# Kernel optimization log

Measured on AMD Instinct MI355X. Metric: run time of the kernel, lower is better.

The kernel has to match this reference:

```python
import jax, jax.numpy as jnp
import numpy as np

HID = 64  # GRU hidden size fixed in source: layers.GRU(64, ...)


def setup_inputs() -> dict:
    key = jax.random.key(0)
    ks = jax.random.split(key, 9)
    B, T, D, K = 128, 1024, 128, 32
    s = 0.05
    X = jax.random.normal(ks[0], (B, T, D), jnp.float32)
    mask = jnp.ones((B, T), jnp.int32)  # 1 = valid token
    # Keras GRU (reset_after=True) params
    gru_kernel = jax.random.normal(ks[1], (D, 3 * HID), jnp.float32) * s
    gru_rec_kernel = jax.random.normal(ks[2], (HID, 3 * HID), jnp.float32) * s
    gru_bias = jax.random.normal(ks[3], (2, 3 * HID), jnp.float32) * s  # [input_bias, recurrent_bias]
    # tfa.layers.CRF params: dense projection + chain kernel + boundary energies
    dense_kernel = jax.random.normal(ks[4], (HID, K), jnp.float32) * s
    dense_bias = jax.random.normal(ks[5], (K,), jnp.float32) * s
    chain_kernel = jax.random.normal(ks[6], (K, K), jnp.float32) * s
    left_boundary = jax.random.normal(ks[7], (K,), jnp.float32) * s
    right_boundary = jax.random.normal(ks[8], (K,), jnp.float32) * s
    return {"X": X, "mask": mask, "gru_kernel": gru_kernel,
            "gru_rec_kernel": gru_rec_kernel, "gru_bias": gru_bias,
            "dense_kernel": dense_kernel, "dense_bias": dense_bias,
            "chain_kernel": chain_kernel, "left_boundary": left_boundary,
            "right_boundary": right_boundary}


def gru_forward(X, mask_bool, gru_kernel, gru_rec_kernel, gru_bias):
    # Keras GRU, reset_after=True: z/r/h gate ordering, tanh/sigmoid activations.
    B, T, D = X.shape
    xproj = X @ gru_kernel + gru_bias[0]  # [B,T,3H] input projection (fused GEMM)

    def step(h, inp):
        xp, mt = inp  # xp: [B,3H], mt: [B] bool
        rec = h @ gru_rec_kernel + gru_bias[1]  # [B,3H]
        xz, xr, xh = jnp.split(xp, 3, axis=-1)
        rz, rr, rh = jnp.split(rec, 3, axis=-1)
        z = jax.nn.sigmoid(xz + rz)
        r = jax.nn.sigmoid(xr + rr)
        hh = jnp.tanh(xh + r * rh)
        hn = z * h + (1.0 - z) * hh
        hn = jnp.where(mt[:, None], hn, h)  # masked steps carry state
        return hn, hn

    h0 = jnp.zeros((B, HID), X.dtype)
    _, hs = jax.lax.scan(step, h0, (jnp.swapaxes(xproj, 0, 1), jnp.swapaxes(mask_bool, 0, 1)))
    return jnp.swapaxes(hs, 0, 1)  # [B,T,H]


def viterbi_decode(potentials, chain_kernel):
    # Max-plus DP with backpointers; potentials: [B,T,K]
    pots = jnp.swapaxes(potentials, 0, 1)  # [T,B,K]

    def fwd(score, pot_t):
        s = score[:, :, None] + chain_kernel[None]  # [B,K_from,K_to]
        bp = jnp.argmax(s, axis=1).astype(jnp.int32)  # [B,K]
        new_score = jnp.max(s, axis=1) + pot_t
        return new_score, bp

    final_score, bps = jax.lax.scan(fwd, pots[0], pots[1:])  # bps: [T-1,B,K]
    last_tag = jnp.argmax(final_score, axis=-1).astype(jnp.int32)  # [B]

    def back(tag, bp):
        prev = jnp.take_along_axis(bp, tag[:, None], axis=1)[:, 0]
        return prev, tag

    first_tag, tags = jax.lax.scan(back, last_tag, bps, reverse=True)  # tags[t] = tag at step t+1
    decoded = jnp.concatenate([first_tag[None], tags], axis=0)  # [T,B]
    return jnp.swapaxes(decoded, 0, 1)  # [B,T]


def reference(X, mask, gru_kernel, gru_rec_kernel, gru_bias,
              dense_kernel, dense_bias, chain_kernel,
              left_boundary, right_boundary):
    B, T, D = X.shape
    mask_bool = mask == 1
    hidden = gru_forward(X, mask_bool, gru_kernel, gru_rec_kernel, gru_bias)
    potentials = hidden @ dense_kernel + dense_bias  # [B,T,K] emissions
    seq_len = jnp.sum(mask, axis=1).astype(jnp.int32)  # [B]
    # Boundary energies (tfa CRF use_boundary=True): left at t=0, right at last valid step
    potentials = potentials.at[:, 0].add(left_boundary)
    potentials = potentials.at[jnp.arange(B), seq_len - 1].add(right_boundary)
    decoded = viterbi_decode(potentials, chain_kernel)  # [B,T] int32
    return decoded, potentials, seq_len, chain_kernel
```

## Files before the change

kernel.cpp:

```cpp
#include <hip/hip_runtime.h>
#include <math.h>

#define BB 128
#define TT 1024
#define DD 128
#define HH 64
#define G3 192
#define KK 32
#define CH 32

__global__ __launch_bounds__(256, 2) void xproj_kernel(const float* __restrict__ X,
                                                       const float* __restrict__ Wk,
                                                       const float* __restrict__ gbias,
                                                       float* __restrict__ xp) {
    __shared__ float Xs[64 * 132];
    __shared__ float Ws[128 * 68];
    const int tid = threadIdx.x;
    const int row0 = blockIdx.x * 64;
    const int cg = blockIdx.y;
#pragma unroll
    for (int it = 0; it < 8; ++it) {
        int idx = it * 1024 + tid * 4;
        int r = idx >> 7, c = idx & 127;
        float4 v = *(const float4*)&X[((size_t)(row0 + r)) * DD + c];
        *(float4*)&Xs[r * 132 + c] = v;
    }
#pragma unroll
    for (int it = 0; it < 8; ++it) {
        int idx = it * 1024 + tid * 4;
        int k = idx >> 6, c = idx & 63;
        float4 v = *(const float4*)&Wk[(size_t)k * G3 + cg * 64 + c];
        *(float4*)&Ws[k * 68 + c] = v;
    }
    __syncthreads();
    const int tr = tid >> 4, tc = tid & 15;
    const int r0 = tr * 4, c0 = tc * 4;
    float acc[4][4];
#pragma unroll
    for (int r = 0; r < 4; ++r)
#pragma unroll
        for (int c = 0; c < 4; ++c) acc[r][c] = 0.f;
#pragma unroll 4
    for (int k = 0; k < DD; k += 4) {
        float a[4][4];
#pragma unroll
        for (int r = 0; r < 4; ++r) {
            float4 t = *(const float4*)&Xs[(r0 + r) * 132 + k];
            a[r][0] = t.x; a[r][1] = t.y; a[r][2] = t.z; a[r][3] = t.w;
        }
#pragma unroll
        for (int kk = 0; kk < 4; ++kk) {
            float4 b = *(const float4*)&Ws[(k + kk) * 68 + c0];
#pragma unroll
            for (int r = 0; r < 4; ++r) {
                acc[r][0] += a[r][kk] * b.x;
                acc[r][1] += a[r][kk] * b.y;
                acc[r][2] += a[r][kk] * b.z;
                acc[r][3] += a[r][kk] * b.w;
            }
        }
    }
    float4 bias = *(const float4*)&gbias[cg * 64 + c0];
#pragma unroll
    for (int r = 0; r < 4; ++r) {
        float4 o;
        o.x = acc[r][0] + bias.x; o.y = acc[r][1] + bias.y;
        o.z = acc[r][2] + bias.z; o.w = acc[r][3] + bias.w;
        *(float4*)&xp[((size_t)(row0 + r0 + r)) * G3 + cg * 64 + c0] = o;
    }
}

#define BCAST(v, l) __int_as_float(__builtin_amdgcn_readlane(__float_as_int(v), (l)))

__global__ __launch_bounds__(320, 1)
void fused_kernel(const float* __restrict__ xp,
                  const float* __restrict__ Wr,
                  const float* __restrict__ gbias,
                  const int* __restrict__ mask,
                  const float* __restrict__ Dk,
                  const float* __restrict__ db,
                  const float* __restrict__ chain,
                  const float* __restrict__ lb,
                  const float* __restrict__ rb,
                  float* __restrict__ out_pot,
                  float* __restrict__ out_dec,
                  float* __restrict__ out_slen,
                  float* __restrict__ out_chn) {
    const int b = blockIdx.x;
    const int tid = threadIdx.x;
    const int w = tid >> 6;
    const int l = tid & 63;
    const int bTT = b * TT;

    __shared__ unsigned char bp[(TT - 1) * KK];
    __shared__ unsigned char table[32 * 32 * KK];
    __shared__ int ent[32];
    __shared__ int last_tag_s;
    __shared__ float gbuf[2][4 * HH];
    __shared__ __align__(16) float hbuf[4][HH];
    __shared__ __align__(16) float potring[64][KK];
    __shared__ __align__(16) float xpstage[2][CH * G3];
    __shared__ int maskst[2][CH];

    if (w < 3) {
        const int j = l;
        float wg[HH];
#pragma unroll
        for (int i2 = 0; i2 < HH; ++i2) wg[i2] = Wr[i2 * G3 + w * HH + j];
#pragma unroll
        for (int i2 = 0; i2 < HH; ++i2) asm volatile("" : "+v"(wg[i2]));
        const float bw = gbias[G3 + w * HH + j];
        __builtin_amdgcn_s_setprio(1);
        float h = 0.f;
        __syncthreads();
        float xv0 = xpstage[0][tid];
        int m0 = maskst[0][0];
        for (int i = 0; i < TT + 2; ++i) {
            if (i < TT) {
                float a0 = bw, a1 = 0.f, a2 = 0.f, a3 = 0.f;
#pragma unroll
                for (int c = 0; c < HH; c += 4) {
                    a0 += BCAST(h, c + 0) * wg[c + 0];
                    a1 += BCAST(h, c + 1) * wg[c + 1];
                    a2 += BCAST(h, c + 2) * wg[c + 2];
                    a3 += BCAST(h, c + 3) * wg[c + 3];
                }
                float a = (a0 + a1) + (a2 + a3);
                float g = (w == 2) ? a : 1.f / (1.f + __expf(-(xv0 + a)));
                gbuf[i & 1][w * HH + j] = g;
                if (w == 2) gbuf[i & 1][3 * HH + j] = xv0;
            }
            __syncthreads();
            if (i < TT) {
                float z  = gbuf[i & 1][j];
                float r  = gbuf[i & 1][HH + j];
                float rh = gbuf[i & 1][2 * HH + j];
                float xh = gbuf[i & 1][3 * HH + j];
                float y = xh + r * rh;
                float hh = 1.f - 2.f / (1.f + __expf(2.f * y));
                float hn = z * h + (1.f - z) * hh;
                hn = (m0 != 0) ? hn : h;
                h = hn;
                if (w == 0) hbuf[i & 3][j] = hn;
                if (i < TT - 1) {
                    const int t1 = i + 1;
                    xv0 = xpstage[(t1 >> 5) & 1][(t1 & 31) * G3 + tid];
                    m0  = maskst[(t1 >> 5) & 1][t1 & 31];
                }
            }
        }
    } else if (w == 3) {
        const int k = l & 31;
        int sl = 0;
#pragma unroll
        for (int q = 0; q < 16; ++q) sl += mask[bTT + q * 64 + l];
#pragma unroll
        for (int d = 32; d >= 1; d >>= 1) sl += __shfl_xor(sl, d, 64);
        if (l == 0) out_slen[b] = (float)sl;
        float dk[HH];
#pragma unroll
        for (int i2 = 0; i2 < HH; ++i2) dk[i2] = Dk[i2 * KK + k];
#pragma unroll
        for (int i2 = 0; i2 < HH; ++i2) asm volatile("" : "+v"(dk[i2]));
        const float dbk = db[k], lbk = lb[k], rbk = rb[k];
        const float* xpg = xp + (size_t)bTT * G3;
        float* potg = out_pot + (size_t)bTT * KK;
#pragma unroll
        for (int q = 0; q < 24; ++q) {
            float4 v = *(const float4*)&xpg[q * 256 + l * 4];
            *(float4*)&xpstage[0][q * 256 + l * 4] = v;
        }
        if (l < CH) maskst[0][l] = mask[bTT + l];
        __syncthreads();
        for (int i = 0; i < TT + 2; ++i) {
            if ((i & 31) == 0) {
                const int cn = (i >> 5) + 1;
                if (cn < 32) {
                    const float* src = xpg + (size_t)cn * CH * G3;
                    float* dst = &xpstage[cn & 1][0];
#pragma unroll
                    for (int q = 0; q < 24; ++q) {
                        float4 v = *(const float4*)&src[q * 256 + l * 4];
                        *(float4*)&dst[q * 256 + l * 4] = v;
                    }
                    if (l < CH) maskst[cn & 1][l] = mask[bTT + cn * CH + l];
                }
                const int cf = (i >> 5) - 2;
                if (cf >= 0) {
                    const float* srcl = &potring[(cf & 1) * 32][0];
                    float* dstg = potg + (size_t)cf * CH * KK;
#pragma unroll
                    for (int q = 0; q < 4; ++q) {
                        float4 v = *(const float4*)&srcl[q * 256 + l * 4];
                        *(float4*)&dstg[q * 256 + l * 4] = v;
                    }
                }
            }
            const int t = i - 2;
            if (t >= 0 && t < TT) {
                const float4* hv4 = (const float4*)&hbuf[t & 3][0];
                float p0 = dbk, p1 = 0.f, p2 = 0.f, p3 = 0.f;
#pragma unroll
                for (int c = 0; c < 16; ++c) {
                    float4 hv = hv4[c];
                    p0 += hv.x * dk[4 * c + 0];
                    p1 += hv.y * dk[4 * c + 1];
                    p2 += hv.z * dk[4 * c + 2];
                    p3 += hv.w * dk[4 * c + 3];
                }
                float pot = (p0 + p1) + (p2 + p3);
                if (t == 0) pot += lbk;
                if (t == sl - 1) pot += rbk;
                if (l < 32) potring[t & 63][k] = pot;
            }
            __syncthreads();
        }
        {
            const float* srcl = &potring[(31 & 1) * 32][0];
            float* dstg = potg + (size_t)31 * CH * KK;
#pragma unroll
            for (int q = 0; q < 4; ++q) {
                float4 v = *(const float4*)&srcl[q * 256 + l * 4];
                *(float4*)&dstg[q * 256 + l * 4] = v;
            }
        }
    } else {
        const int k = l & 31;
        const int hf = l >> 5;
        float ccol[16];
        int addr[16];
#pragma unroll
        for (int m = 0; m < 16; ++m) {
            ccol[m] = chain[(hf * 16 + m) * KK + k];
            addr[m] = (hf * 16 + m) * 4;
        }
#pragma unroll
        for (int m = 0; m < 16; ++m) asm volatile("" : "+v"(ccol[m]));
        const int addrx = (l ^ 32) * 4;
        float s = 0.f;
        __syncthreads();
        for (int i = 0; i < TT + 2; ++i) {
            __syncthreads();
            const int t = i - 2;
            if (t >= 0 && t < TT) {
                float pot = potring[t & 63][k];
                if (t == 0) {
                    s = pot;
                } else {
                    const int si = __float_as_int(s);
                    float c[16];
#pragma unroll
                    for (int m = 0; m < 16; ++m)
                        c[m] = __int_as_float(__builtin_amdgcn_ds_bpermute(addr[m], si)) + ccol[m];
                    float v1[8]; int i1[8];
#pragma unroll
                    for (int p = 0; p < 8; ++p) {
                        bool tk = c[2 * p + 1] > c[2 * p];
                        v1[p] = tk ? c[2 * p + 1] : c[2 * p];
                        i1[p] = hf * 16 + (tk ? 2 * p + 1 : 2 * p);
                    }
                    float v2[4]; int i2[4];
#pragma unroll
                    for (int p = 0; p < 4; ++p) {
                        bool tk = v1[2 * p + 1] > v1[2 * p];
                        v2[p] = tk ? v1[2 * p + 1] : v1[2 * p];
                        i2[p] = tk ? i1[2 * p + 1] : i1[2 * p];
                    }
                    float v3[2]; int i3[2];
#pragma unroll
                    for (int p = 0; p < 2; ++p) {
                        bool tk = v2[2 * p + 1] > v2[2 * p];
                        v3[p] = tk ? v2[2 * p + 1] : v2[2 * p];
                        i3[p] = tk ? i2[2 * p + 1] : i2[2 * p];
                    }
                    bool tk = v3[1] > v3[0];
                    float bv = tk ? v3[1] : v3[0];
                    int bi = tk ? i3[1] : i3[0];
                    float ov = __int_as_float(__builtin_amdgcn_ds_bpermute(addrx, __float_as_int(bv)));
                    int   oi = __builtin_amdgcn_ds_bpermute(addrx, bi);
                    bool take = (ov > bv) || (ov == bv && oi < bi);
                    if (take) { bv = ov; bi = oi; }
                    if (l < 32) bp[(t - 1) * KK + k] = (unsigned char)bi;
                    s = bv + pot;
                }
            }
        }
        float bv = s; int bi = k;
#pragma unroll
        for (int d = 16; d >= 1; d >>= 1) {
            float ov = __shfl_xor(bv, d, 64);
            int   oi = __shfl_xor(bi, d, 64);
            bool take = (ov > bv) || (ov == bv && oi < bi);
            if (take) { bv = ov; bi = oi; }
        }
        if (l == 0) last_tag_s = bi;
    }
    __syncthreads();
    {
        const int k = tid & 31;
        const int grp = tid >> 5;
        for (int c = grp; c < 32; c += 10) {
            int tag = k;
            for (int ll = 31; ll >= 0; --ll) {
                const int t = c * 32 + ll;
                if (t < TT - 1) tag = bp[t * KK + tag];
                table[(c * 32 + ll) * KK + k] = (unsigned char)tag;
            }
        }
    }
    __syncthreads();
    if (tid == 0) {
        int e = last_tag_s;
        ent[31] = e;
        for (int c = 30; c >= 0; --c) { e = table[(c + 1) * 32 * KK + e]; ent[c] = e; }
    }
    __syncthreads();
    for (int t = tid; t < TT; t += 320) {
        const int c = t >> 5, ll = t & 31;
        out_dec[(size_t)bTT + t] = (float)table[(c * 32 + ll) * KK + ent[c]];
    }
    if (b == 0) {
        for (int i2 = tid; i2 < KK * KK; i2 += 320) out_chn[i2] = chain[i2];
    }
}

extern "C" void kernel_launch(void* const* d_in, const int* in_sizes, int n_in,
                              void* d_out, int out_size, void* d_ws, size_t ws_size,
                              hipStream_t stream) {
    const float* X     = (const float*)d_in[0];
    const int*   mask  = (const int*)d_in[1];
    const float* Wk    = (const float*)d_in[2];
    const float* Wr    = (const float*)d_in[3];
    const float* gb    = (const float*)d_in[4];
    const float* Dk    = (const float*)d_in[5];
    const float* db    = (const float*)d_in[6];
    const float* chain = (const float*)d_in[7];
    const float* lb    = (const float*)d_in[8];
    const float* rb    = (const float*)d_in[9];

    float* out = (float*)d_out;
    float* out_dec  = out;
    float* out_pot  = out + (size_t)BB * TT;
    float* out_slen = out + (size_t)BB * TT + (size_t)BB * TT * KK;
    float* out_chn  = out_slen + BB;

    float* xp = (float*)d_ws;

    xproj_kernel<<<dim3((BB * TT) / 64, 3), dim3(256), 0, stream>>>(X, Wk, gb, xp);
    fused_kernel<<<dim3(BB), dim3(320), 0, stream>>>(xp, Wr, gb, mask, Dk, db, chain,
                                                     lb, rb, out_pot, out_dec,
                                                     out_slen, out_chn);
}
```

Measured before the change: 898.2 us.

## Split GRU and Viterbi into separate blocks linked by global-memory chunk flags

Launches twice as many blocks: the first 128 run the GRU recurrence and emission projection, writing potentials to global memory and raising a per-chunk flag. The other 128 spin-wait on those flags, stage each potential chunk into shared memory and run the Viterbi forward pass and backtrace. This takes the Viterbi wave out of the GRU block's per-step barrier, so the recurrence no longer waits on it. The cost is inter-block producer/consumer synchronisation through global atomics, which assumes all 256 blocks are resident at once to avoid deadlock, plus flag resets at the end of each call.

```diff
diff --git a/kernel.cpp b/kernel.cpp
--- a/kernel.cpp
+++ b/kernel.cpp
@@ -8,6 +8,10 @@
 #define G3 192
 #define KK 32
 #define CH 32
+
+#define BCAST(v, l) __int_as_float(__builtin_amdgcn_readlane(__float_as_int(v), (l)))
+
+__device__ int g_pflags[BB * 32];
 
 __global__ __launch_bounds__(256, 2) void xproj_kernel(const float* __restrict__ X,
                                                        const float* __restrict__ Wk,
@@ -70,165 +74,188 @@
     }
 }
 
-#define BCAST(v, l) __int_as_float(__builtin_amdgcn_readlane(__float_as_int(v), (l)))
-
-__global__ __launch_bounds__(320, 1)
-void fused_kernel(const float* __restrict__ xp,
-                  const float* __restrict__ Wr,
-                  const float* __restrict__ gbias,
-                  const int* __restrict__ mask,
-                  const float* __restrict__ Dk,
-                  const float* __restrict__ db,
-                  const float* __restrict__ chain,
-                  const float* __restrict__ lb,
-                  const float* __restrict__ rb,
-                  float* __restrict__ out_pot,
-                  float* __restrict__ out_dec,
-                  float* __restrict__ out_slen,
-                  float* __restrict__ out_chn) {
-    const int b = blockIdx.x;
+__global__ __launch_bounds__(256, 1)
+void gruvit_kernel(const float* __restrict__ xp,
+                   const float* __restrict__ Wr,
+                   const float* __restrict__ gbias,
+                   const int* __restrict__ mask,
+                   const float* __restrict__ Dk,
+                   const float* __restrict__ db,
+                   const float* __restrict__ chain,
+                   const float* __restrict__ lb,
+                   const float* __restrict__ rb,
+                   float* __restrict__ out_pot,
+                   float* __restrict__ out_dec,
+                   float* __restrict__ out_slen,
+                   float* __restrict__ out_chn) {
+    __shared__ __align__(16) unsigned char smem[73856];
     const int tid = threadIdx.x;
     const int w = tid >> 6;
     const int l = tid & 63;
+
+    if (blockIdx.x < BB) {
+        const int b = blockIdx.x;
+        const int bTT = b * TT;
+        float (*gbuf)[4 * HH]     = (float (*)[4 * HH])(smem);
+        float (*hbuf)[HH]         = (float (*)[HH])(smem + 2048);
+        float (*potring)[KK]      = (float (*)[KK])(smem + 3072);
+        float (*xpstage)[CH * G3] = (float (*)[CH * G3])(smem + 11264);
+        int (*maskst)[CH]         = (int (*)[CH])(smem + 60416);
+
+        if (w < 3) {
+            const int j = l;
+            float wg[HH];
+#pragma unroll
+            for (int i2 = 0; i2 < HH; ++i2) wg[i2] = Wr[i2 * G3 + w * HH + j];
+#pragma unroll
+            for (int i2 = 0; i2 < HH; ++i2) asm volatile("" : "+v"(wg[i2]));
+            const float bw = gbias[G3 + w * HH + j];
+            __builtin_amdgcn_s_setprio(1);
+            float h = 0.f;
+            __syncthreads();
+            float xv0 = xpstage[0][tid];
+            int m0 = maskst[0][0];
+            for (int i = 0; i < TT + 2; ++i) {
+                if (i < TT) {
+                    float a0 = bw, a1 = 0.f, a2 = 0.f, a3 = 0.f;
+#pragma unroll
+                    for (int c = 0; c < HH; c += 4) {
+                        a0 += BCAST(h, c + 0) * wg[c + 0];
+                        a1 += BCAST(h, c + 1) * wg[c + 1];
+                        a2 += BCAST(h, c + 2) * wg[c + 2];
+                        a3 += BCAST(h, c + 3) * wg[c + 3];
+                    }
+                    float a = (a0 + a1) + (a2 + a3);
+                    float g = (w == 2) ? a : 1.f / (1.f + __expf(-(xv0 + a)));
+                    gbuf[i & 1][w * HH + j] = g;
+                    if (w == 2) gbuf[i & 1][3 * HH + j] = xv0;
+                }
+                __syncthreads();
+                if (i < TT) {
+                    float z  = gbuf[i & 1][j];
+                    float r  = gbuf[i & 1][HH + j];
+                    float rh = gbuf[i & 1][2 * HH + j];
+                    float xh = gbuf[i & 1][3 * HH + j];
+                    float y = xh + r * rh;
+                    float hh = 1.f - 2.f / (1.f + __expf(2.f * y));
+                    float hn = z * h + (1.f - z) * hh;
+                    hn = (m0 != 0) ? hn : h;
+                    h = hn;
+                    if (w == 0) hbuf[i & 3][j] = hn;
+                    if (i < TT - 1) {
+                        const int t1 = i + 1;
+                        xv0 = xpstage[(t1 >> 5) & 1][(t1 & 31) * G3 + tid];
+                        m0  = maskst[(t1 >> 5) & 1][t1 & 31];
+                    }
+                }
+            }
+        } else {
+            const int k = l & 31;
+            int sl = 0;
+#pragma unroll
+            for (int q = 0; q < 16; ++q) sl += mask[bTT + q * 64 + l];
+#pragma unroll
+            for (int d = 32; d >= 1; d >>= 1) sl += __shfl_xor(sl, d, 64);
+            if (l == 0) out_slen[b] = (float)sl;
+            float dk[HH];
+#pragma unroll
+            for (int i2 = 0; i2 < HH; ++i2) dk[i2] = Dk[i2 * KK + k];
+#pragma unroll
+            for (int i2 = 0; i2 < HH; ++i2) asm volatile("" : "+v"(dk[i2]));
+            const float dbk = db[k], lbk = lb[k], rbk = rb[k];
+            const float* xpg = xp + (size_t)bTT * G3;
+            float* potg = out_pot + (size_t)bTT * KK;
+#pragma unroll
+            for (int q = 0; q < 24; ++q) {
+                float4 v = *(const float4*)&xpg[q * 256 + l * 4];
+                *(float4*)&xpstage[0][q * 256 + l * 4] = v;
+            }
+            if (l < CH) maskst[0][l] = mask[bTT + l];
+            __syncthreads();
+            for (int i = 0; i < TT + 2; ++i) {
+                if ((i & 31) == 0) {
+                    const int cn = (i >> 5) + 1;
+                    if (cn < 32) {
+                        const float* src = xpg + (size_t)cn * CH * G3;
+                        float* dst = &xpstage[cn & 1][0];
+#pragma unroll
+                        for (int q = 0; q < 24; ++q) {
+                            float4 v = *(const float4*)&src[q * 256 + l * 4];
+                            *(float4*)&dst[q * 256 + l * 4] = v;
+                        }
+                        if (l < CH) maskst[cn & 1][l] = mask[bTT + cn * CH + l];
+                    }
+                    const int cf = (i >> 5) - 2;
+                    if (cf >= 0) {
+                        const float* srcl = &potring[(cf & 1) * 32][0];
+                        float* dstg = potg + (size_t)cf * CH * KK;
+#pragma unroll
+                        for (int q = 0; q < 4; ++q) {
+                            float4 v = *(const float4*)&srcl[q * 256 + l * 4];
+                            *(float4*)&dstg[q * 256 + l * 4] = v;
+                        }
+                    }
+                }
+                if ((i & 31) == 4 && l == 0) {
+                    const int cp = (i >> 5) - 2;
+                    if (cp >= 0) {
+                        __threadfence();
+                        atomicExch(&g_pflags[b * 32 + cp], 1);
+                    }
+                }
+                const int t = i - 2;
+                if (t >= 0 && t < TT) {
+                    const float4* hv4 = (const float4*)&hbuf[t & 3][0];
+                    float p0 = dbk, p1 = 0.f, p2 = 0.f, p3 = 0.f;
+#pragma unroll
+                    for (int c = 0; c < 16; ++c) {
+                        float4 hv = hv4[c];
+                        p0 += hv.x * dk[4 * c + 0];
+                        p1 += hv.y * dk[4 * c + 1];
+                        p2 += hv.z * dk[4 * c + 2];
+                        p3 += hv.w * dk[4 * c + 3];
+                    }
+                    float pot = (p0 + p1) + (p2 + p3);
+                    if (t == 0) pot += lbk;
+                    if (t == sl - 1) pot += rbk;
+                    if (l < 32) potring[t & 63][k] = pot;
+                }
+                __syncthreads();
+            }
+            {
+                const float* srcl = &potring[(31 & 1) * 32][0];
+                float* dstg = potg + (size_t)31 * CH * KK;
+#pragma unroll
+                for (int q = 0; q < 4; ++q) {
+                    float4 v = *(const float4*)&srcl[q * 256 + l * 4];
+                    *(float4*)&dstg[q * 256 + l * 4] = v;
+                }
+                if (l == 0) {
+                    __threadfence();
+                    atomicExch(&g_pflags[b * 32 + 30], 1);
+                    atomicExch(&g_pflags[b * 32 + 31], 1);
+                }
+            }
+        }
+        return;
+    }
+
+    const int b = blockIdx.x - BB;
     const int bTT = b * TT;
-
-    __shared__ unsigned char bp[(TT - 1) * KK];
-    __shared__ unsigned char table[32 * 32 * KK];
-    __shared__ int ent[32];
-    __shared__ int last_tag_s;
-    __shared__ float gbuf[2][4 * HH];
-    __shared__ __align__(16) float hbuf[4][HH];
-    __shared__ __align__(16) float potring[64][KK];
-    __shared__ __align__(16) float xpstage[2][CH * G3];
-    __shared__ int maskst[2][CH];
-
-    if (w < 3) {
-        const int j = l;
-        float wg[HH];
-#pragma unroll
-        for (int i2 = 0; i2 < HH; ++i2) wg[i2] = Wr[i2 * G3 + w * HH + j];
-#pragma unroll
-        for (int i2 = 0; i2 < HH; ++i2) asm volatile("" : "+v"(wg[i2]));
-        const float bw = gbias[G3 + w * HH + j];
-        __builtin_amdgcn_s_setprio(1);
-        float h = 0.f;
-        __syncthreads();
-        float xv0 = xpstage[0][tid];
-        int m0 = maskst[0][0];
-        for (int i = 0; i < TT + 2; ++i) {
-            if (i < TT) {
-                float a0 = bw, a1 = 0.f, a2 = 0.f, a3 = 0.f;
-#pragma unroll
-                for (int c = 0; c < HH; c += 4) {
-                    a0 += BCAST(h, c + 0) * wg[c + 0];
-                    a1 += BCAST(h, c + 1) * wg[c + 1];
-                    a2 += BCAST(h, c + 2) * wg[c + 2];
-                    a3 += BCAST(h, c + 3) * wg[c + 3];
-                }
-                float a = (a0 + a1) + (a2 + a3);
-                float g = (w == 2) ? a : 1.f / (1.f + __expf(-(xv0 + a)));
-                gbuf[i & 1][w * HH + j] = g;
-                if (w == 2) gbuf[i & 1][3 * HH + j] = xv0;
-            }
-            __syncthreads();
-            if (i < TT) {
-                float z  = gbuf[i & 1][j];
-                float r  = gbuf[i & 1][HH + j];
-                float rh = gbuf[i & 1][2 * HH + j];
-                float xh = gbuf[i & 1][3 * HH + j];
-                float y = xh + r * rh;
-                float hh = 1.f - 2.f / (1.f + __expf(2.f * y));
-                float hn = z * h + (1.f - z) * hh;
-                hn = (m0 != 0) ? hn : h;
-                h = hn;
-                if (w == 0) hbuf[i & 3][j] = hn;
-                if (i < TT - 1) {
-                    const int t1 = i + 1;
-                    xv0 = xpstage[(t1 >> 5) & 1][(t1 & 31) * G3 + tid];
-                    m0  = maskst[(t1 >> 5) & 1][t1 & 31];
-                }
-            }
-        }
-    } else if (w == 3) {
-        const int k = l & 31;
-        int sl = 0;
-#pragma unroll
-        for (int q = 0; q < 16; ++q) sl += mask[bTT + q * 64 + l];
-#pragma unroll
-        for (int d = 32; d >= 1; d >>= 1) sl += __shfl_xor(sl, d, 64);
-        if (l == 0) out_slen[b] = (float)sl;
-        float dk[HH];
-#pragma unroll
-        for (int i2 = 0; i2 < HH; ++i2) dk[i2] = Dk[i2 * KK + k];
-#pragma unroll
-        for (int i2 = 0; i2 < HH; ++i2) asm volatile("" : "+v"(dk[i2]));
-        const float dbk = db[k], lbk = lb[k], rbk = rb[k];
-        const float* xpg = xp + (size_t)bTT * G3;
-        float* potg = out_pot + (size_t)bTT * KK;
-#pragma unroll
-        for (int q = 0; q < 24; ++q) {
-            float4 v = *(const float4*)&xpg[q * 256 + l * 4];
-            *(float4*)&xpstage[0][q * 256 + l * 4] = v;
-        }
-        if (l < CH) maskst[0][l] = mask[bTT + l];
-        __syncthreads();
-        for (int i = 0; i < TT + 2; ++i) {
-            if ((i & 31) == 0) {
-                const int cn = (i >> 5) + 1;
-                if (cn < 32) {
-                    const float* src = xpg + (size_t)cn * CH * G3;
-                    float* dst = &xpstage[cn & 1][0];
-#pragma unroll
-                    for (int q = 0; q < 24; ++q) {
-                        float4 v = *(const float4*)&src[q * 256 + l * 4];
-                        *(float4*)&dst[q * 256 + l * 4] = v;
-                    }
-                    if (l < CH) maskst[cn & 1][l] = mask[bTT + cn * CH + l];
-                }
-                const int cf = (i >> 5) - 2;
-                if (cf >= 0) {
-                    const float* srcl = &potring[(cf & 1) * 32][0];
-                    float* dstg = potg + (size_t)cf * CH * KK;
-#pragma unroll
-                    for (int q = 0; q < 4; ++q) {
-                        float4 v = *(const float4*)&srcl[q * 256 + l * 4];
-                        *(float4*)&dstg[q * 256 + l * 4] = v;
-                    }
-                }
-            }
-            const int t = i - 2;
-            if (t >= 0 && t < TT) {
-                const float4* hv4 = (const float4*)&hbuf[t & 3][0];
-                float p0 = dbk, p1 = 0.f, p2 = 0.f, p3 = 0.f;
-#pragma unroll
-                for (int c = 0; c < 16; ++c) {
-                    float4 hv = hv4[c];
-                    p0 += hv.x * dk[4 * c + 0];
-                    p1 += hv.y * dk[4 * c + 1];
-                    p2 += hv.z * dk[4 * c + 2];
-                    p3 += hv.w * dk[4 * c + 3];
-                }
-                float pot = (p0 + p1) + (p2 + p3);
-                if (t == 0) pot += lbk;
-                if (t == sl - 1) pot += rbk;
-                if (l < 32) potring[t & 63][k] = pot;
-            }
-            __syncthreads();
-        }
-        {
-            const float* srcl = &potring[(31 & 1) * 32][0];
-            float* dstg = potg + (size_t)31 * CH * KK;
-#pragma unroll
-            for (int q = 0; q < 4; ++q) {
-                float4 v = *(const float4*)&srcl[q * 256 + l * 4];
-                *(float4*)&dstg[q * 256 + l * 4] = v;
-            }
-        }
-    } else {
-        const int k = l & 31;
-        const int hf = l >> 5;
-        float ccol[16];
-        int addr[16];
+    const float* potg = out_pot + (size_t)bTT * KK;
+    const int k = l & 31;
+    const int hf = l >> 5;
+    const int addrx = (l ^ 32) * 4;
+
+    unsigned char* bp    = smem;
+    unsigned char* table = smem + 32736;
+    float (*potbuf)[CH][KK] = (float (*)[CH][KK])(smem + 65504);
+    int* ent        = (int*)(smem + 73696);
+    int* last_tag_s = (int*)(smem + 73824);
+
+    float ccol[16];
+    int addr[16];
+    if (w == 1) {
 #pragma unroll
         for (int m = 0; m < 16; ++m) {
             ccol[m] = chain[(hf * 16 + m) * KK + k];
@@ -236,27 +263,51 @@
         }
 #pragma unroll
         for (int m = 0; m < 16; ++m) asm volatile("" : "+v"(ccol[m]));
-        const int addrx = (l ^ 32) * 4;
-        float s = 0.f;
-        __syncthreads();
-        for (int i = 0; i < TT + 2; ++i) {
-            __syncthreads();
-            const int t = i - 2;
-            if (t >= 0 && t < TT) {
-                float pot = potring[t & 63][k];
+    }
+    if (w == 0) {
+        if (l == 0) {
+            while (atomicAdd(&g_pflags[b * 32 + 0], 0) == 0) __builtin_amdgcn_s_sleep(8);
+        }
+        __threadfence();
+#pragma unroll
+        for (int q = 0; q < 4; ++q) {
+            float4 v = *(const float4*)&potg[(size_t)(q * 64 + l) * 4];
+            ((float4*)&potbuf[0][0][0])[q * 64 + l] = v;
+        }
+    }
+    __syncthreads();
+    float s = 0.f;
+    for (int c = 0; c < 32; ++c) {
+        if (w == 0 && c + 1 < 32) {
+            if (l == 0) {
+                while (atomicAdd(&g_pflags[b * 32 + c + 1], 0) == 0)
+                    __builtin_amdgcn_s_sleep(8);
+            }
+            __threadfence();
+            const float* src = potg + (size_t)(c + 1) * CH * KK;
+#pragma unroll
+            for (int q = 0; q < 4; ++q) {
+                float4 v = *(const float4*)&src[(size_t)(q * 64 + l) * 4];
+                ((float4*)&potbuf[(c + 1) & 1][0][0])[q * 64 + l] = v;
+            }
+        }
+        if (w == 1) {
+            for (int ll = 0; ll < 32; ++ll) {
+                const int t = c * 32 + ll;
+                float pot = potbuf[c & 1][ll][k];
                 if (t == 0) {
                     s = pot;
                 } else {
                     const int si = __float_as_int(s);
-                    float c[16];
+                    float cc[16];
 #pragma unroll
                     for (int m = 0; m < 16; ++m)
-                        c[m] = __int_as_float(__builtin_amdgcn_ds_bpermute(addr[m], si)) + ccol[m];
+                        cc[m] = __int_as_float(__builtin_amdgcn_ds_bpermute(addr[m], si)) + ccol[m];
                     float v1[8]; int i1[8];
 #pragma unroll
                     for (int p = 0; p < 8; ++p) {
-                        bool tk = c[2 * p + 1] > c[2 * p];
-                        v1[p] = tk ? c[2 * p + 1] : c[2 * p];
+                        bool tk = cc[2 * p + 1] > cc[2 * p];
+                        v1[p] = tk ? cc[2 * p + 1] : cc[2 * p];
                         i1[p] = hf * 16 + (tk ? 2 * p + 1 : 2 * p);
                     }
                     float v2[4]; int i2[4];
@@ -285,6 +336,9 @@
                 }
             }
         }
+        __syncthreads();
+    }
+    if (w == 1) {
         float bv = s; int bi = k;
 #pragma unroll
         for (int d = 16; d >= 1; d >>= 1) {
@@ -293,35 +347,36 @@
             bool take = (ov > bv) || (ov == bv && oi < bi);
             if (take) { bv = ov; bi = oi; }
         }
-        if (l == 0) last_tag_s = bi;
+        if (l == 0) *last_tag_s = bi;
     }
     __syncthreads();
     {
-        const int k = tid & 31;
+        const int kk2 = tid & 31;
         const int grp = tid >> 5;
-        for (int c = grp; c < 32; c += 10) {
-            int tag = k;
+        for (int c = grp; c < 32; c += 8) {
+            int tag = kk2;
             for (int ll = 31; ll >= 0; --ll) {
                 const int t = c * 32 + ll;
                 if (t < TT - 1) tag = bp[t * KK + tag];
-                table[(c * 32 + ll) * KK + k] = (unsigned char)tag;
+                table[(c * 32 + ll) * KK + kk2] = (unsigned char)tag;
             }
         }
     }
     __syncthreads();
     if (tid == 0) {
-        int e = last_tag_s;
+        int e = *last_tag_s;
         ent[31] = e;
         for (int c = 30; c >= 0; --c) { e = table[(c + 1) * 32 * KK + e]; ent[c] = e; }
     }
     __syncthreads();
-    for (int t = tid; t < TT; t += 320) {
+    for (int t = tid; t < TT; t += 256) {
         const int c = t >> 5, ll = t & 31;
         out_dec[(size_t)bTT + t] = (float)table[(c * 32 + ll) * KK + ent[c]];
     }
-    if (b == 0) {
-        for (int i2 = tid; i2 < KK * KK; i2 += 320) out_chn[i2] = chain[i2];
-    }
+    if (blockIdx.x == BB) {
+        for (int i2 = tid; i2 < KK * KK; i2 += 256) out_chn[i2] = chain[i2];
+    }
+    for (int i2 = tid; i2 < 32; i2 += 256) atomicExch(&g_pflags[b * 32 + i2], 0);
 }
 
 extern "C" void kernel_launch(void* const* d_in, const int* in_sizes, int n_in,
@@ -347,7 +402,7 @@
     float* xp = (float*)d_ws;
 
     xproj_kernel<<<dim3((BB * TT) / 64, 3), dim3(256), 0, stream>>>(X, Wk, gb, xp);
-    fused_kernel<<<dim3(BB), dim3(320), 0, stream>>>(xp, Wr, gb, mask, Dk, db, chain,
-                                                     lb, rb, out_pot, out_dec,
-                                                     out_slen, out_chn);
+    gruvit_kernel<<<dim3(2 * BB), dim3(256), 0, stream>>>(xp, Wr, gb, mask, Dk, db,
+                                                          chain, lb, rb, out_pot,
+                                                          out_dec, out_slen, out_chn);
 }
```

New measurement: 745.9 us. -17.0%, faster.
